# Optimization experiments

Measured on AMD Instinct MI355X. Metric: run time of the kernel, lower is better.

The kernel has to match this reference:

```python
import jax, jax.numpy as jnp
import numpy as np

N, H, W, CIN, COUT, FSIZE = 8, 128, 128, 64, 128, 3
EPS = 1e-3      # keras BatchNormalization default epsilon
ALPHA = 0.2     # LeakyReLU alpha


def setup_inputs() -> dict:
    key = jax.random.key(0)
    k0, k1, k2 = jax.random.split(key, 3)
    return {
        "inputs_real": jax.random.normal(k0, (N, H, W, CIN), jnp.float32),
        "inputs_imag": jax.random.normal(k1, (N, H, W, CIN), jnp.float32),
        "filters": jax.random.normal(k2, (FSIZE, FSIZE, CIN, COUT), jnp.float32) * 0.1,
        "gamma_real": jnp.ones((COUT,), jnp.float32),
        "beta_real": jnp.zeros((COUT,), jnp.float32),
        "gamma_imag": jnp.ones((COUT,), jnp.float32),
        "beta_imag": jnp.zeros((COUT,), jnp.float32),
    }


def _bn_train(x, gamma, beta):
    # BatchNorm in training mode: batch stats over (N, H, W), biased variance.
    mean = jnp.mean(x, axis=(0, 1, 2), keepdims=True)
    var = jnp.var(x, axis=(0, 1, 2), keepdims=True)
    return gamma * (x - mean) * jax.lax.rsqrt(var + EPS) + beta


def _leaky(x):
    return jnp.where(x >= 0, x, ALPHA * x)


def _spectral_kernels(filters):
    # Pad spatial filters [f,f,Cin,Cout] to [H,W,Cin,Cout] (bottom/right), FFT over H,W.
    f = filters.shape[0]
    fp = jnp.pad(filters, ((0, H - f), (0, W - f), (0, 0), (0, 0)))
    ff = jnp.fft.fft2(jnp.transpose(fp, (2, 3, 0, 1)).astype(jnp.complex64))  # [Cin,Cout,H,W]
    ff = jnp.transpose(ff, (2, 3, 0, 1))  # [H,W,Cin,Cout]
    kr = jnp.real(ff)
    ki = jnp.real(ff)  # faithful to source: filters_imag is ALSO tf.math.real(filters_freq)
    return kr, ki


def reference(inputs_real, inputs_imag, filters, gamma_real, beta_real, gamma_imag, beta_imag):
    kr, ki = _spectral_kernels(filters)
    # Fused form of the per-batch loop: sum over Cin of (ac+bd) and (bc-ad).
    out_real = (jnp.einsum('nhwc,hwco->nhwo', inputs_real, kr)
                + jnp.einsum('nhwc,hwco->nhwo', inputs_imag, ki))
    out_imag = (jnp.einsum('nhwc,hwco->nhwo', inputs_imag, kr)
                - jnp.einsum('nhwc,hwco->nhwo', inputs_real, ki))
    out_real = _leaky(_bn_train(out_real, gamma_real, beta_real))
    out_imag = _leaky(_bn_train(out_imag, gamma_imag, beta_imag))
    return (out_real, out_imag)
```

## Files before the change

### kernel.cpp

```cpp
#include <hip/hip_runtime.h>
#include <hip/hip_bf16.h>


typedef __bf16 bf16x8 __attribute__((ext_vector_type(8)));
typedef float f32x4 __attribute__((ext_vector_type(4)));

__device__ __forceinline__ unsigned pack2(float a, float b) {
    __hip_bfloat162 h = __float22bfloat162_rn(make_float2(a, b));
    return *reinterpret_cast<unsigned*>(&h);
}
__device__ __forceinline__ void unpack8(uint4 u, float* f) {
    f[0] = __uint_as_float(u.x << 16); f[1] = __uint_as_float(u.x & 0xffff0000u);
    f[2] = __uint_as_float(u.y << 16); f[3] = __uint_as_float(u.y & 0xffff0000u);
    f[4] = __uint_as_float(u.z << 16); f[5] = __uint_as_float(u.z & 0xffff0000u);
    f[6] = __uint_as_float(u.w << 16); f[7] = __uint_as_float(u.w & 0xffff0000u);
}

__global__ __launch_bounds__(512, 4) void conv_stats(
    const float* __restrict__ xr, const float* __restrict__ xi,
    const float* __restrict__ filt, float* __restrict__ out,
    float* __restrict__ gstats)
{
    __shared__ __align__(16) unsigned short pqT[5 * 4096];
    __shared__ __align__(16) unsigned short xsh[16 * 16 * 64];
    __shared__ float statl[512];

    const int t = threadIdx.x;
    const int gid = blockIdx.x;
    const int oh = gid >> 8;
    const int u  = (gid & 255) >> 1;
    const int vh = gid & 1;
    const int obase = oh << 6;
    const int vbase0 = vh << 6;

    unsigned* pq32 = (unsigned*)pqT;
    unsigned* xs32 = (unsigned*)xsh;

    const float au = 6.28318530717958647692f * (float)u / 128.0f;
    float su1, cu1, su2, cu2;
    __sincosf(au, &su1, &cu1);
    __sincosf(2.0f * au, &su2, &cu2);

    #pragma unroll
    for (int k = 0; k < 4; ++k) {
        int i = t + k * 512;
        int o = i & 63;
        int cp = i >> 6;
        int g0 = (2 * cp) * 128 + obase + o;
        int g1 = g0 + 128;
        unsigned wd = o * 32 + (((cp >> 2) ^ (o & 7)) << 2) + (cp & 3);
        #pragma unroll
        for (int b = 0; b < 3; ++b) {
            float f0a = filt[b * 8192 + g0],       f0b = filt[b * 8192 + g1];
            float f1a = filt[(3 + b) * 8192 + g0], f1b = filt[(3 + b) * 8192 + g1];
            float f2a = filt[(6 + b) * 8192 + g0], f2b = filt[(6 + b) * 8192 + g1];
            float Pa = fmaf(cu2, f2a, fmaf(cu1, f1a, f0a));
            float Pb = fmaf(cu2, f2b, fmaf(cu1, f1b, f0b));
            pq32[b * 2048 + wd] = pack2(Pa, Pb);
            if (b > 0) {
                float Qa = fmaf(su2, f2a, su1 * f1a);
                float Qb = fmaf(su2, f2b, su1 * f1b);
                pq32[(b + 2) * 2048 + wd] = pack2(Qa, Qb);
            }
        }
    }

    const int wave = t >> 6;
    const int lane = t & 63;
    const int vg   = wave >> 1;
    const int nth  = wave & 1;
    const int ln15 = lane & 15;
    const int q    = lane >> 4;
    const int swz  = ln15 & 7;
    const int part = q >> 1;
    const int nbase = (q & 1) * 4;

    const int sv = t >> 5;
    const int scp = t & 31;

    float ssum[2] = {0.f, 0.f}, ssq[2] = {0.f, 0.f};

    #pragma unroll 1
    for (int ch = 0; ch < 4; ++ch) {
        {
            const int vglob = vbase0 + ch * 16 + sv;
            unsigned wb = (sv * 16) * 32 + (((scp >> 2) ^ 0) << 2) + (scp & 3);
            #pragma unroll
            for (int n = 0; n < 8; ++n) {
                size_t gi = (((size_t)(n * 128 + u)) * 128 + vglob) * 64 + 2 * scp;
                float2 r  = *(const float2*)(xr + gi);
                float2 m2 = *(const float2*)(xi + gi);
                unsigned rp = pack2(r.x + m2.x, r.y + m2.y);
                unsigned ip = pack2(m2.x - r.x, m2.y - r.y);
                unsigned base = (sv * 16 + n) * 32 + (((scp >> 2) ^ (n & 7)) << 2) + (scp & 3);
                xs32[base] = rp;
                xs32[base + 8 * 32] = ip;
            }
            (void)wb;
        }
        __syncthreads();

        float cv1[4], cv2[4], nsv1[4], nsv2[4];
        #pragma unroll
        for (int vj = 0; vj < 4; ++vj) {
            float av = 6.28318530717958647692f *
                       (float)(vbase0 + ch * 16 + vg * 4 + vj) / 128.0f;
            float s1, c1, s2, c2;
            __sincosf(av, &s1, &c1);
            __sincosf(2.0f * av, &s2, &c2);
            cv1[vj] = c1; cv2[vj] = c2; nsv1[vj] = -s1; nsv2[vj] = -s2;
        }

        bf16x8 af[4][2];
        #pragma unroll
        for (int vj = 0; vj < 4; ++vj) {
            const unsigned short* xrow = &xsh[((vg * 4 + vj) * 16 + ln15) * 64];
            #pragma unroll
            for (int ks = 0; ks < 2; ++ks) {
                int m = ks * 4 + q;
                af[vj][ks] = __builtin_bit_cast(bf16x8,
                    *(const uint4*)(xrow + ((m ^ swz) << 3)));
            }
        }

        #pragma unroll
        for (int ntl = 0; ntl < 2; ++ntl) {
            const int ot = nth * 2 + ntl;
            const int o_loc = ot * 16 + ln15;
            const unsigned short* prow = &pqT[o_loc * 64];
            f32x4 acc[4];
            #pragma unroll
            for (int vj = 0; vj < 4; ++vj) acc[vj] = (f32x4){0.f, 0.f, 0.f, 0.f};

            #pragma unroll
            for (int ks = 0; ks < 2; ++ks) {
                const int m = ks * 4 + q;
                const int foff = (m ^ swz) << 3;
                float P0[8], P1[8], P2[8], Q1[8], Q2[8];
                unpack8(*(const uint4*)(prow + 0 * 4096 + foff), P0);
                unpack8(*(const uint4*)(prow + 1 * 4096 + foff), P1);
                unpack8(*(const uint4*)(prow + 2 * 4096 + foff), P2);
                unpack8(*(const uint4*)(prow + 3 * 4096 + foff), Q1);
                unpack8(*(const uint4*)(prow + 4 * 4096 + foff), Q2);
                #pragma unroll
                for (int vj = 0; vj < 4; ++vj) {
                    float kr[8];
                    #pragma unroll
                    for (int j = 0; j < 8; ++j) {
                        float tv = fmaf(cv1[vj], P1[j], P0[j]);
                        tv = fmaf(cv2[vj], P2[j], tv);
                        tv = fmaf(nsv1[vj], Q1[j], tv);
                        kr[j] = fmaf(nsv2[vj], Q2[j], tv);
                    }
                    uint4 B;
                    B.x = pack2(kr[0], kr[1]); B.y = pack2(kr[2], kr[3]);
                    B.z = pack2(kr[4], kr[5]); B.w = pack2(kr[6], kr[7]);
                    acc[vj] = __builtin_amdgcn_mfma_f32_16x16x32_bf16(
                        af[vj][ks], __builtin_bit_cast(bf16x8, B), acc[vj], 0, 0, 0);
                }
            }

            const int o_glob = obase + o_loc;
            #pragma unroll
            for (int vj = 0; vj < 4; ++vj) {
                const int vglob = vbase0 + ch * 16 + vg * 4 + vj;
                size_t base = (size_t)part * 16777216 + (size_t)nbase * 2097152
                            + ((size_t)(u * 128 + vglob)) * 128 + o_glob;
                #pragma unroll
                for (int r = 0; r < 4; ++r) {
                    float y = acc[vj][r];
                    out[base + (size_t)r * 2097152] = y;
                    ssum[ntl] += y;
                    ssq[ntl] = fmaf(y, y, ssq[ntl]);
                }
            }
        }
        __syncthreads();
    }

    statl[t] = 0.f;
    __syncthreads();
    #pragma unroll
    for (int ntl = 0; ntl < 2; ++ntl) {
        int chn = part * 128 + obase + (nth * 2 + ntl) * 16 + ln15;
        atomicAdd(&statl[chn], ssum[ntl]);
        atomicAdd(&statl[256 + chn], ssq[ntl]);
    }
    __syncthreads();
    atomicAdd(&gstats[t], statl[t]);
}

__global__ void bn_prep(const float* __restrict__ gstats,
                        const float* __restrict__ gr, const float* __restrict__ br,
                        const float* __restrict__ gi, const float* __restrict__ bi,
                        float* __restrict__ sc_sh)
{
    int t = threadIdx.x;
    if (t < 256) {
        int part = t >> 7, o = t & 127;
        const float inv = 1.0f / 131072.0f;
        float mean = gstats[t] * inv;
        float var  = gstats[256 + t] * inv - mean * mean;
        float g = part ? gi[o] : gr[o];
        float b = part ? bi[o] : br[o];
        float s = g * rsqrtf(var + 1e-3f);
        sc_sh[t]       = s;
        sc_sh[256 + t] = b - mean * s;
    }
}

__global__ __launch_bounds__(256) void bn_apply(float* __restrict__ out,
                                                const float* __restrict__ sc_sh)
{
    size_t base = (size_t)blockIdx.x * 256 + threadIdx.x;
    #pragma unroll
    for (int it = 0; it < 4; ++it, base += (size_t)8192 * 256) {
        size_t e = base * 4;
        int part = (int)(e >> 24);
        int o = (int)(e & 127);
        const f32x4 sc = *(const f32x4*)(sc_sh + part * 128 + o);
        const f32x4 sh = *(const f32x4*)(sc_sh + 256 + part * 128 + o);
        f32x4 x = *(const f32x4*)(out + e);
        f32x4 y;
        y[0] = fmaf(x[0], sc[0], sh[0]);
        y[1] = fmaf(x[1], sc[1], sh[1]);
        y[2] = fmaf(x[2], sc[2], sh[2]);
        y[3] = fmaf(x[3], sc[3], sh[3]);
        x[0] = y[0] >= 0.0f ? y[0] : 0.2f * y[0];
        x[1] = y[1] >= 0.0f ? y[1] : 0.2f * y[1];
        x[2] = y[2] >= 0.0f ? y[2] : 0.2f * y[2];
        x[3] = y[3] >= 0.0f ? y[3] : 0.2f * y[3];
        __builtin_nontemporal_store(x, (f32x4*)(out + e));
    }
}

extern "C" void kernel_launch(void* const* d_in, const int* in_sizes, int n_in,
                              void* d_out, int out_size, void* d_ws, size_t ws_size,
                              hipStream_t stream)
{
    const float* xr   = (const float*)d_in[0];
    const float* xi   = (const float*)d_in[1];
    const float* filt = (const float*)d_in[2];
    const float* gr   = (const float*)d_in[3];
    const float* br   = (const float*)d_in[4];
    const float* gi   = (const float*)d_in[5];
    const float* bi   = (const float*)d_in[6];
    float* out = (float*)d_out;
    float* ws  = (float*)d_ws;

    (void)hipMemsetAsync(ws, 0, 512 * sizeof(float), stream);
    conv_stats<<<dim3(512), dim3(512), 0, stream>>>(xr, xi, filt, out, ws);
    bn_prep<<<dim3(1), dim3(256), 0, stream>>>(ws, gr, br, gi, bi, ws + 512);
    bn_apply<<<dim3(8192), dim3(256), 0, stream>>>(out, ws + 512);
}
```

Before: 311.2 us.

## Apply twiddle combination after MFMA and prefetch next input chunk

The spectral weight is no longer built per output column as a bf16 combination of five partial filter planes before each MFMA. The kernel now runs five MFMAs against the raw P0/P1/P2/Q1/Q2 planes and combines the fp32 accumulators with cos/sin twiddles afterward, which removes the per-element unpack, FMA and pack work. In exchange it issues five times as many MFMAs per tile. The input chunk loads are also software-pipelined into registers one chunk ahead, so global loads overlap compute, at the cost of extra registers and a changed barrier placement.

```diff
diff --git a/kernel.cpp b/kernel.cpp
--- a/kernel.cpp
+++ b/kernel.cpp
@@ -8,12 +8,6 @@
 __device__ __forceinline__ unsigned pack2(float a, float b) {
     __hip_bfloat162 h = __float22bfloat162_rn(make_float2(a, b));
     return *reinterpret_cast<unsigned*>(&h);
-}
-__device__ __forceinline__ void unpack8(uint4 u, float* f) {
-    f[0] = __uint_as_float(u.x << 16); f[1] = __uint_as_float(u.x & 0xffff0000u);
-    f[2] = __uint_as_float(u.y << 16); f[3] = __uint_as_float(u.y & 0xffff0000u);
-    f[4] = __uint_as_float(u.z << 16); f[5] = __uint_as_float(u.z & 0xffff0000u);
-    f[6] = __uint_as_float(u.w << 16); f[7] = __uint_as_float(u.w & 0xffff0000u);
 }
 
 __global__ __launch_bounds__(512, 4) void conv_stats(
@@ -78,105 +72,97 @@
     const int sv = t >> 5;
     const int scp = t & 31;
 
+    float2 rr[8], ri[8];
+    auto LOADX = [&](int chk) {
+        const int vglob = vbase0 + chk * 16 + sv;
+        #pragma unroll
+        for (int n = 0; n < 8; ++n) {
+            size_t gi = (((size_t)(n * 128 + u)) * 128 + vglob) * 64 + 2 * scp;
+            rr[n] = *(const float2*)(xr + gi);
+            ri[n] = *(const float2*)(xi + gi);
+        }
+    };
+    auto STOREX = [&]() {
+        #pragma unroll
+        for (int n = 0; n < 8; ++n) {
+            unsigned rp = pack2(rr[n].x + ri[n].x, rr[n].y + ri[n].y);
+            unsigned ip = pack2(ri[n].x - rr[n].x, ri[n].y - rr[n].y);
+            unsigned base = (sv * 16 + n) * 32 + (((scp >> 2) ^ (n & 7)) << 2) + (scp & 3);
+            xs32[base] = rp;
+            xs32[base + 8 * 32] = ip;
+        }
+    };
+
     float ssum[2] = {0.f, 0.f}, ssq[2] = {0.f, 0.f};
 
+    LOADX(0);
+
     #pragma unroll 1
-    for (int ch = 0; ch < 4; ++ch) {
-        {
-            const int vglob = vbase0 + ch * 16 + sv;
-            unsigned wb = (sv * 16) * 32 + (((scp >> 2) ^ 0) << 2) + (scp & 3);
-            #pragma unroll
-            for (int n = 0; n < 8; ++n) {
-                size_t gi = (((size_t)(n * 128 + u)) * 128 + vglob) * 64 + 2 * scp;
-                float2 r  = *(const float2*)(xr + gi);
-                float2 m2 = *(const float2*)(xi + gi);
-                unsigned rp = pack2(r.x + m2.x, r.y + m2.y);
-                unsigned ip = pack2(m2.x - r.x, m2.y - r.y);
-                unsigned base = (sv * 16 + n) * 32 + (((scp >> 2) ^ (n & 7)) << 2) + (scp & 3);
-                xs32[base] = rp;
-                xs32[base + 8 * 32] = ip;
-            }
-            (void)wb;
-        }
+    for (int chk = 0; chk < 4; ++chk) {
+        __syncthreads();
+        STOREX();
+        if (chk < 3) LOADX(chk + 1);
         __syncthreads();
 
         float cv1[4], cv2[4], nsv1[4], nsv2[4];
         #pragma unroll
         for (int vj = 0; vj < 4; ++vj) {
             float av = 6.28318530717958647692f *
-                       (float)(vbase0 + ch * 16 + vg * 4 + vj) / 128.0f;
+                       (float)(vbase0 + chk * 16 + vg * 4 + vj) / 128.0f;
             float s1, c1, s2, c2;
             __sincosf(av, &s1, &c1);
             __sincosf(2.0f * av, &s2, &c2);
             cv1[vj] = c1; cv2[vj] = c2; nsv1[vj] = -s1; nsv2[vj] = -s2;
         }
 
-        bf16x8 af[4][2];
-        #pragma unroll
-        for (int vj = 0; vj < 4; ++vj) {
-            const unsigned short* xrow = &xsh[((vg * 4 + vj) * 16 + ln15) * 64];
+        #pragma unroll
+        for (int ntl = 0; ntl < 2; ++ntl) {
+            const int o_loc = (nth * 2 + ntl) * 16 + ln15;
+            const unsigned short* prow = &pqT[o_loc * 64];
+
+            bf16x8 pf[2][5];
             #pragma unroll
             for (int ks = 0; ks < 2; ++ks) {
-                int m = ks * 4 + q;
-                af[vj][ks] = __builtin_bit_cast(bf16x8,
-                    *(const uint4*)(xrow + ((m ^ swz) << 3)));
+                const int foff = (((ks * 4 + q) ^ swz) << 3);
+                #pragma unroll
+                for (int p = 0; p < 5; ++p)
+                    pf[ks][p] = __builtin_bit_cast(bf16x8,
+                        *(const uint4*)(prow + p * 4096 + foff));
             }
-        }
-
-        #pragma unroll
-        for (int ntl = 0; ntl < 2; ++ntl) {
-            const int ot = nth * 2 + ntl;
-            const int o_loc = ot * 16 + ln15;
-            const unsigned short* prow = &pqT[o_loc * 64];
-            f32x4 acc[4];
-            #pragma unroll
-            for (int vj = 0; vj < 4; ++vj) acc[vj] = (f32x4){0.f, 0.f, 0.f, 0.f};
-
-            #pragma unroll
-            for (int ks = 0; ks < 2; ++ks) {
-                const int m = ks * 4 + q;
-                const int foff = (m ^ swz) << 3;
-                float P0[8], P1[8], P2[8], Q1[8], Q2[8];
-                unpack8(*(const uint4*)(prow + 0 * 4096 + foff), P0);
-                unpack8(*(const uint4*)(prow + 1 * 4096 + foff), P1);
-                unpack8(*(const uint4*)(prow + 2 * 4096 + foff), P2);
-                unpack8(*(const uint4*)(prow + 3 * 4096 + foff), Q1);
-                unpack8(*(const uint4*)(prow + 4 * 4096 + foff), Q2);
-                #pragma unroll
-                for (int vj = 0; vj < 4; ++vj) {
-                    float kr[8];
-                    #pragma unroll
-                    for (int j = 0; j < 8; ++j) {
-                        float tv = fmaf(cv1[vj], P1[j], P0[j]);
-                        tv = fmaf(cv2[vj], P2[j], tv);
-                        tv = fmaf(nsv1[vj], Q1[j], tv);
-                        kr[j] = fmaf(nsv2[vj], Q2[j], tv);
-                    }
-                    uint4 B;
-                    B.x = pack2(kr[0], kr[1]); B.y = pack2(kr[2], kr[3]);
-                    B.z = pack2(kr[4], kr[5]); B.w = pack2(kr[6], kr[7]);
-                    acc[vj] = __builtin_amdgcn_mfma_f32_16x16x32_bf16(
-                        af[vj][ks], __builtin_bit_cast(bf16x8, B), acc[vj], 0, 0, 0);
-                }
-            }
-
-            const int o_glob = obase + o_loc;
+
             #pragma unroll
             for (int vj = 0; vj < 4; ++vj) {
-                const int vglob = vbase0 + ch * 16 + vg * 4 + vj;
+                const unsigned short* xrow = &xsh[((vg * 4 + vj) * 16 + ln15) * 64];
+                bf16x8 af0 = __builtin_bit_cast(bf16x8,
+                    *(const uint4*)(xrow + ((q ^ swz) << 3)));
+                bf16x8 af1 = __builtin_bit_cast(bf16x8,
+                    *(const uint4*)(xrow + (((4 + q) ^ swz) << 3)));
+
+                f32x4 tp[5];
+                #pragma unroll
+                for (int p = 0; p < 5; ++p) {
+                    f32x4 z = (f32x4){0.f, 0.f, 0.f, 0.f};
+                    z = __builtin_amdgcn_mfma_f32_16x16x32_bf16(af0, pf[0][p], z, 0, 0, 0);
+                    tp[p] = __builtin_amdgcn_mfma_f32_16x16x32_bf16(af1, pf[1][p], z, 0, 0, 0);
+                }
+
+                const int vglob = vbase0 + chk * 16 + vg * 4 + vj;
                 size_t base = (size_t)part * 16777216 + (size_t)nbase * 2097152
-                            + ((size_t)(u * 128 + vglob)) * 128 + o_glob;
+                            + ((size_t)(u * 128 + vglob)) * 128 + obase + o_loc;
                 #pragma unroll
                 for (int r = 0; r < 4; ++r) {
-                    float y = acc[vj][r];
+                    float y = fmaf(cv1[vj], tp[1][r], tp[0][r]);
+                    y = fmaf(cv2[vj], tp[2][r], y);
+                    y = fmaf(nsv1[vj], tp[3][r], y);
+                    y = fmaf(nsv2[vj], tp[4][r], y);
                     out[base + (size_t)r * 2097152] = y;
                     ssum[ntl] += y;
                     ssq[ntl] = fmaf(y, y, ssq[ntl]);
                 }
             }
         }
-        __syncthreads();
-    }
+    }
+    __syncthreads();
 
     statl[t] = 0.f;
     __syncthreads();
```

Result: slower. 475.5 us (+52.8%).
